# Kernel tuning notes

Measured on AMD Instinct MI355X. Metric: run time of the kernel, lower is better.

The kernel has to match this reference:

```python
import jax, jax.numpy as jnp
import numpy as np

B, T, C, H, HD = 2, 1024, 1024, 16, 64

def _l2norm(x):
    return x / jnp.maximum(jnp.linalg.norm(x, axis=-1, keepdims=True), 1e-12)

def _rms(x):
    return x * jax.lax.rsqrt(jnp.mean(x * x, axis=-1, keepdims=True) + 1e-6)

def _rope_tables(t, hd):
    inv = 1.0 / (10000.0 ** (jnp.arange(0, hd, 2, dtype=jnp.float32) / hd))
    fr = jnp.outer(jnp.arange(t, dtype=jnp.float32), inv)  # [T, hd/2]
    return jnp.cos(fr)[None, :, None, :], jnp.sin(fr)[None, :, None, :]

def _rope(x, cos, sin):
    h = x.shape[-1] // 2
    x1, x2 = x[..., :h], x[..., h:]
    return jnp.concatenate([x1 * cos + x2 * sin, -x1 * sin + x2 * cos], axis=-1)

def _qkv_heads(x, Wqkv, cos, sin):
    q, k, v = jnp.split(x @ Wqkv.T, 3, axis=-1)
    q = _rope(q.reshape(B, T, H, HD), cos, sin)
    k = _rope(k.reshape(B, T, H, HD), cos, sin)
    return q, k, v.reshape(B, T, H, HD)

def _bhtd(x):
    return jnp.swapaxes(x, 1, 2)

def _sdpa(q, k, v, scale, causal):
    s = jnp.einsum('bhqd,bhkd->bhqk', q, k) * scale
    s = jnp.where(causal, s, -jnp.inf)
    return jnp.einsum('bhqk,bhkd->bhqd', jax.nn.softmax(s, axis=-1), v)

def _hyp_attn(q, k, v, kc, causal):
    # project to Lorentz hyperboloid <x,x>_L = -k: time = sqrt(k + |x_s|^2)
    tq = jnp.sqrt(kc + jnp.sum(q * q, axis=-1, keepdims=True))  # [B,H,T,1]
    tk = jnp.sqrt(kc + jnp.sum(k * k, axis=-1, keepdims=True))
    # Lorentz inner product for all pairs, via GEMM (no [B,H,T,T,D+1] blowup)
    inner = jnp.einsum('bhqd,bhkd->bhqk', q, k) - tq * jnp.swapaxes(tk, -1, -2)
    # d(x,y) = sqrt(k) * arccosh(-<x,y>_L / k); clamp arg for numerical safety
    dist = jnp.sqrt(kc) * jnp.arccosh(jnp.maximum(-inner / kc, 1.0 + 1e-7))
    w = jnp.where(causal, 1.0 / (1e-6 + dist), -jnp.inf)
    return jnp.einsum('bhqk,bhkd->bhqd', jax.nn.softmax(w, axis=-1), v)

def _mlp(x, Wuv, Wmo, suv_eff=None):
    uv = x @ Wuv.T
    if suv_eff is not None:
        uv = suv_eff * uv
    u, v = jnp.split(uv, 2, axis=-1)
    return (u * jax.nn.silu(v)) @ Wmo.T

def _sph_skip(x, h, alpha):
    lr = jnp.abs(alpha * (0.05 * (C ** 0.5)))  # alpha * (init_value/init_scaling)
    a, b = _l2norm(x), _l2norm(h)
    return _l2norm(a + lr * (b - a))

def _euc_hyp_block(x, Wqkv, Wo, Wuv, Wmo, cos, sin, causal, kc=None):
    h = _rms(x)
    q, k, v = _qkv_heads(h, Wqkv, cos, sin)
    q, k, v = _bhtd(q), _bhtd(k), _bhtd(v)
    if kc is None:
        a = _sdpa(q, k, v, 1.0 / (C ** 0.5), causal)
    else:
        a = _hyp_attn(q, k, v, kc, causal)
    x = x + _bhtd(a).reshape(B, T, C) @ Wo.T
    x = x + _mlp(_rms(x), Wuv, Wmo)
    return x

def _sph_block(x, Wqkv, Wo, Wuv, Wmo, sqk, suv, attn_alpha, mlp_alpha, cos, sin, causal):
    q, k, v = _qkv_heads(x, Wqkv, cos, sin)
    sqk_eff = (sqk * (C ** 0.5)).reshape(1, 1, H, HD)  # sqk * init_value/init_scaling
    q = sqk_eff * _l2norm(q)
    k = sqk_eff * _l2norm(k)
    a = _sdpa(_bhtd(q), _bhtd(k), _bhtd(v), C ** 0.5, causal)
    x = _sph_skip(x, _bhtd(a).reshape(B, T, C) @ Wo.T, attn_alpha)
    x = _sph_skip(x, _mlp(x, Wuv, Wmo, suv_eff=suv * (C ** 0.5)), mlp_alpha)
    return x

def setup_inputs() -> dict:
    key = jax.random.key(0)
    ks = jax.random.split(key, 14)
    w = lambda k, shp: jax.random.normal(k, shp, jnp.float32) * 0.02
    inp = {'x': jax.random.normal(ks[0], (B, T, C), jnp.float32)}
    for i, g in enumerate(['euc', 'hyp', 'sph']):
        inp[f'Wqkv_{g}'] = w(ks[1 + 4 * i], (3 * C, C))
        inp[f'Wo_{g}'] = w(ks[2 + 4 * i], (C, C))
        inp[f'Wuv_{g}'] = w(ks[3 + 4 * i], (8 * C, C))
        inp[f'Wmo_{g}'] = w(ks[4 + 4 * i], (C, 4 * C))
    inp['k_hyp'] = jnp.ones((1, H, 1, 1), jnp.float32)
    inp['sqk'] = jnp.ones((C,), jnp.float32) / (C ** 0.5)
    inp['suv'] = jnp.ones((8 * C,), jnp.float32)
    inp['attn_alpha'] = jnp.ones((C,), jnp.float32) / (C ** 0.5)
    inp['mlp_alpha'] = jnp.ones((C,), jnp.float32) / (C ** 0.5)
    return inp

def reference(x, Wqkv_euc, Wo_euc, Wuv_euc, Wmo_euc,
              Wqkv_hyp, Wo_hyp, Wuv_hyp, Wmo_hyp, k_hyp,
              Wqkv_sph, Wo_sph, Wuv_sph, Wmo_sph,
              sqk, suv, attn_alpha, mlp_alpha):
    cos, sin = _rope_tables(T, HD)
    causal = jnp.tril(jnp.ones((T, T), dtype=bool))
    x = _euc_hyp_block(x, Wqkv_euc, Wo_euc, Wuv_euc, Wmo_euc, cos, sin, causal)
    x = _euc_hyp_block(x, Wqkv_hyp, Wo_hyp, Wuv_hyp, Wmo_hyp, cos, sin, causal, kc=k_hyp)
    x = _sph_block(x, Wqkv_sph, Wo_sph, Wuv_sph, Wmo_sph, sqk, suv, attn_alpha, mlp_alpha, cos, sin, causal)
    return x
```

## Files before the change

### kernel.cpp

```cpp
#include <hip/hip_runtime.h>
#include <stdint.h>
#include <stddef.h>

typedef __attribute__((ext_vector_type(8))) short short8;
typedef __attribute__((ext_vector_type(4))) float f32x4;
typedef unsigned short u16;
typedef unsigned int u32;

#define DEVI __device__ __forceinline__

static constexpr int T_ = 1024, C_ = 1024, M_ = 2048;

DEVI float bf2f(u16 u){ u32 x=((u32)u)<<16; float f; __builtin_memcpy(&f,&x,4); return f; }
DEVI u16 f2bf(float f){ u32 x; __builtin_memcpy(&x,&f,4); x += 0x7fffu + ((x>>16)&1u); return (u16)(x>>16); }

DEVI void gld_lds16(const u16* g, u16* l){
  __builtin_amdgcn_global_load_lds((const __attribute__((address_space(1))) void*)g,
                                   (__attribute__((address_space(3))) void*)l, 16, 0, 0);
}
DEVI f32x4 mfma16(short8 a, short8 b, f32x4 c){
  return __builtin_amdgcn_mfma_f32_16x16x32_bf16(a, b, c, 0, 0, 0);
}

__global__ void k_cast(const float* __restrict__ in, u16* __restrict__ out){
  int i = (blockIdx.x*blockDim.x + threadIdx.x)*4;
  float4 v = *(const float4*)(in+i);
  uint2 o; o.x = (u32)f2bf(v.x) | ((u32)f2bf(v.y)<<16);
  o.y = (u32)f2bf(v.z) | ((u32)f2bf(v.w)<<16);
  *(uint2*)(out+i) = o;
}

__global__ void k_tables(float* __restrict__ cosT, float* __restrict__ sinT){
  int i = blockIdx.x*256 + threadIdx.x;
  int t = i>>5, f = i&31;
  float inv = expf(-((float)f/32.f)*9.210340371976184f);
  float fr = (float)t * inv;
  cosT[i] = cosf(fr); sinT[i] = sinf(fr);
}

template<int NORM>
__global__ void k_rms(const float* __restrict__ x, u16* __restrict__ out){
  __shared__ float ps[4];
  int row = blockIdx.x, tid = threadIdx.x;
  float4 v = ((const float4*)(x + (size_t)row*C_))[tid];
  if (NORM){
    float ss = v.x*v.x+v.y*v.y+v.z*v.z+v.w*v.w;
    #pragma unroll
    for(int o=32;o>=1;o>>=1) ss += __shfl_xor(ss,o);
    if((tid&63)==0) ps[tid>>6]=ss;
    __syncthreads();
    ss = ps[0]+ps[1]+ps[2]+ps[3];
    float r = rsqrtf(ss*(1.f/C_) + 1e-6f);
    v.x*=r; v.y*=r; v.z*=r; v.w*=r;
  }
  uint2 o; o.x=(u32)f2bf(v.x)|((u32)f2bf(v.y)<<16);
  o.y=(u32)f2bf(v.z)|((u32)f2bf(v.w)<<16);
  ((uint2*)(out + (size_t)row*C_))[tid] = o;
}

template<int EPI>
__global__ __launch_bounds__(256) void k_gemm(const u16* __restrict__ A, const u16* __restrict__ Bw,
    void* __restrict__ Cout, const float* __restrict__ Res, int M, int N, int K){
  __shared__ u16 As[128*32];
  __shared__ u16 Bs[128*32];
  const int tid = threadIdx.x, w = tid>>6, lane = tid&63;
  const int bm = blockIdx.y<<7, bn = blockIdx.x<<7;
  const int wr = w>>1, wc = w&1;
  const int sr = lane>>2, sc = lane&3;
  f32x4 acc[4][4] = {};
  const u16* ga0 = A  + (size_t)(bm + w*32 + sr)*K + sc*8;
  const u16* gb0 = Bw + (size_t)(bn + w*32 + sr)*K + sc*8;
  u16* la0 = &As[(w*32)*32];
  u16* lb0 = &Bs[(w*32)*32];
  const int r16 = lane&15, ko = (lane>>4)*8;
  for (int k0=0; k0<K; k0+=32){
    __syncthreads();
    gld_lds16(ga0 + k0, la0);
    gld_lds16(ga0 + (size_t)16*K + k0, la0 + 16*32);
    gld_lds16(gb0 + k0, lb0);
    gld_lds16(gb0 + (size_t)16*K + k0, lb0 + 16*32);
    __syncthreads();
    short8 af[4], bf[4];
    #pragma unroll
    for(int mf=0;mf<4;++mf) af[mf] = *(const short8*)&As[(wr*64+mf*16+r16)*32 + ko];
    #pragma unroll
    for(int nf=0;nf<4;++nf) bf[nf] = *(const short8*)&Bs[(wc*64+nf*16+r16)*32 + ko];
    #pragma unroll
    for(int mf=0;mf<4;++mf)
      #pragma unroll
      for(int nf=0;nf<4;++nf)
        acc[mf][nf] = mfma16(af[mf], bf[nf], acc[mf][nf]);
  }
  const int rr = (lane>>4)*4;
  #pragma unroll
  for(int mf=0;mf<4;++mf){
    #pragma unroll
    for(int nf=0;nf<4;++nf){
      #pragma unroll
      for(int r=0;r<4;++r){
        size_t idx = (size_t)(bm + wr*64 + mf*16 + rr + r)*N + (bn + wc*64 + nf*16 + r16);
        float val = acc[mf][nf][r];
        if (EPI==0)      ((u16*)Cout)[idx] = f2bf(val);
        else if (EPI==1) ((float*)Cout)[idx] = Res[idx] + val;
        else             ((float*)Cout)[idx] = val;
      }
    }
  }
}

template<int SPH>
__global__ void k_ropeqk(const u16* __restrict__ qkv, const float* __restrict__ cosT,
                         const float* __restrict__ sinT, const float* __restrict__ sqk,
                         u16* __restrict__ Qb, u16* __restrict__ Kb){
  int idx = blockIdx.x*4 + (threadIdx.x>>6);
  int lane = threadIdx.x&63;
  int bh = idx>>10, t = idx&1023;
  int b = bh>>4, h = bh&15;
  size_t qa = (size_t)(b*T_ + t)*3072 + h*64 + lane;
  float qv = bf2f(qkv[qa]), kv = bf2f(qkv[qa + 1024]);
  float c = cosT[t*32 + (lane&31)], s = sinT[t*32 + (lane&31)];
  float qo = __shfl(qv, lane^32), ko2 = __shfl(kv, lane^32);
  float qr = (lane<32) ? (qv*c + qo*s) : (qv*c - qo*s);
  float kr = (lane<32) ? (kv*c + ko2*s) : (kv*c - ko2*s);
  if (SPH){
    float sq = qr*qr, sk = kr*kr;
    #pragma unroll
    for(int o=32;o>=1;o>>=1){ sq += __shfl_xor(sq,o); sk += __shfl_xor(sk,o); }
    float sc2 = sqk[h*64+lane]*32.f;
    qr = qr / fmaxf(sqrtf(sq),1e-12f) * sc2;
    kr = kr / fmaxf(sqrtf(sk),1e-12f) * sc2;
  }
  size_t oa = (size_t)bh*T_*64 + (size_t)t*64 + lane;
  Qb[oa] = f2bf(qr); Kb[oa] = f2bf(kr);
}

__global__ void k_vtrans(const u16* __restrict__ qkv, u16* __restrict__ Vt){
  __shared__ u16 tile[64][68];
  int bh = blockIdx.x, t0 = blockIdx.y*64;
  int b = bh>>4, h = bh&15;
  int tid = threadIdx.x;
  int tt = tid>>2, ch = tid&3;
  const u16* src = qkv + (size_t)(b*T_ + t0 + tt)*3072 + 2048 + h*64 + ch*16;
  short8 v0 = *(const short8*)src;
  short8 v1 = *(const short8*)(src+8);
  #pragma unroll
  for(int j=0;j<8;++j){ tile[tt][ch*16+j]=(u16)v0[j]; tile[tt][ch*16+8+j]=(u16)v1[j]; }
  __syncthreads();
  int d = tid>>2, tc = (tid&3)*16;
  short8 a, bb;
  #pragma unroll
  for(int j=0;j<8;++j){ a[j]=(short)tile[tc+j][d]; bb[j]=(short)tile[tc+8+j][d]; }
  u16* dst = Vt + ((size_t)bh*64 + d)*T_ + t0 + tc;
  *(short8*)dst = a; *(short8*)(dst+8) = bb;
}

template<int GEOM>
__global__ __launch_bounds__(64) void k_attn_split(const u16* __restrict__ Q, const u16* __restrict__ K,
    const u16* __restrict__ Vt, const float* __restrict__ khyp,
    float* __restrict__ partO, float* __restrict__ partML){
  int qt = blockIdx.x, bh = blockIdx.y, ch = blockIdx.z;
  int kend = qt*16 + 16;
  int kbeg = ch*256;
  if (kbeg >= kend) return;
  int klim = min(kbeg + 256, kend);
  __shared__ u16 P[16*32];
  int b = bh>>4, h = bh&15;
  int lane = threadIdx.x;
  int r16 = lane&15, g = lane>>4, ko = g*8;
  const u16* Qp = Q + (size_t)bh*T_*64;
  const u16* Kp = K + (size_t)bh*T_*64;
  const u16* Vp = Vt + (size_t)bh*64*T_;
  short8 qf0 = *(const short8*)&Qp[(size_t)(qt*16 + r16)*64 + ko];
  short8 qf1 = *(const short8*)&Qp[(size_t)(qt*16 + r16)*64 + 32 + ko];
  float kc=1.f, sqkc=1.f, tqr[4];
  if (GEOM==1){
    kc = khyp[h]; sqkc = sqrtf(kc);
    float ss=0;
    #pragma unroll
    for(int j=0;j<8;++j){ float a=bf2f((u16)qf0[j]); ss+=a*a; a=bf2f((u16)qf1[j]); ss+=a*a; }
    ss += __shfl_xor(ss,16); ss += __shfl_xor(ss,32);
    float tq = sqrtf(kc + ss);
    #pragma unroll
    for(int r=0;r<4;++r) tqr[r] = __shfl(tq, g*4+r);
  }
  f32x4 of[4] = {};
  float m[4], l[4];
  #pragma unroll
  for(int r=0;r<4;++r){ m[r]=-1e30f; l[r]=0.f; }
  int ntiles = (klim - kbeg + 31)>>5;
  for(int it=0; it<ntiles; ++it){
    int kt = kbeg + it*32;
    short8 kf00 = *(const short8*)&Kp[(size_t)(kt + r16)*64 + ko];
    short8 kf01 = *(const short8*)&Kp[(size_t)(kt + r16)*64 + 32 + ko];
    short8 kf10 = *(const short8*)&Kp[(size_t)(kt + 16 + r16)*64 + ko];
    short8 kf11 = *(const short8*)&Kp[(size_t)(kt + 16 + r16)*64 + 32 + ko];
    f32x4 s0={}, s1={};
    s0 = mfma16(qf0, kf00, s0); s0 = mfma16(qf1, kf01, s0);
    s1 = mfma16(qf0, kf10, s1); s1 = mfma16(qf1, kf11, s1);
    float tk0=0.f, tk1=0.f;
    if (GEOM==1){
      float ss0=0, ss1=0;
      #pragma unroll
      for(int j=0;j<8;++j){
        float a=bf2f((u16)kf00[j]); ss0+=a*a; a=bf2f((u16)kf01[j]); ss0+=a*a;
        a=bf2f((u16)kf10[j]); ss1+=a*a; a=bf2f((u16)kf11[j]); ss1+=a*a;
      }
      ss0 += __shfl_xor(ss0,16); ss0 += __shfl_xor(ss0,32);
      ss1 += __shfl_xor(ss1,16); ss1 += __shfl_xor(ss1,32);
      tk0 = sqrtf(kc+ss0); tk1 = sqrtf(kc+ss1);
    }
    float w0[4], w1[4];
    #pragma unroll
    for(int r=0;r<4;++r){
      int qg = qt*16 + g*4 + r;
      float a0, a1;
      if (GEOM==0){ a0 = s0[r]*(1.f/32.f); a1 = s1[r]*(1.f/32.f); }
      else if (GEOM==2){ a0 = s0[r]*32.f; a1 = s1[r]*32.f; }
      else {
        float z0 = (tqr[r]*tk0 - s0[r])/kc; z0 = fmaxf(z0, 1.f+1e-7f);
        float z1 = (tqr[r]*tk1 - s1[r])/kc; z1 = fmaxf(z1, 1.f+1e-7f);
        float d0 = sqkc * logf(z0 + sqrtf(z0*z0 - 1.f));
        float d1 = sqkc * logf(z1 + sqrtf(z1*z1 - 1.f));
        a0 = 1.f/(1e-6f + d0); a1 = 1.f/(1e-6f + d1);
      }
      if (kt + r16 > qg)      a0 = -1e30f;
      if (kt + 16 + r16 > qg) a1 = -1e30f;
      w0[r]=a0; w1[r]=a1;
    }
    #pragma unroll
    for(int r=0;r<4;++r){
      float mt = fmaxf(w0[r], w1[r]);
      #pragma unroll
      for(int o=1;o<16;o<<=1) mt = fmaxf(mt, __shfl_xor(mt,o));
      float mn = fmaxf(m[r], mt);
      float alpha = __expf(m[r]-mn);
      m[r]=mn;
      float p0 = __expf(w0[r]-mn), p1 = __expf(w1[r]-mn);
      float rs = p0+p1;
      #pragma unroll
      for(int o=1;o<16;o<<=1) rs += __shfl_xor(rs,o);
      l[r] = l[r]*alpha + rs;
      #pragma unroll
      for(int vb=0;vb<4;++vb) of[vb][r] *= alpha;
      P[(g*4+r)*32 + r16]      = f2bf(p0);
      P[(g*4+r)*32 + 16 + r16] = f2bf(p1);
    }
    __syncthreads();
    short8 pf = *(const short8*)&P[r16*32 + ko];
    #pragma unroll
    for(int vb=0;vb<4;++vb){
      short8 vf = *(const short8*)&Vp[(size_t)(vb*16 + r16)*T_ + kt + ko];
      of[vb] = mfma16(pf, vf, of[vb]);
    }
    __syncthreads();
  }
  size_t base = ((size_t)(bh*64 + qt)*4 + ch);
  float* po = partO + base*1024;
  #pragma unroll
  for(int vb=0;vb<4;++vb)
    #pragma unroll
    for(int r=0;r<4;++r)
      po[(g*4+r)*64 + vb*16 + r16] = of[vb][r];
  if (r16 == 0){
    #pragma unroll
    for(int r=0;r<4;++r){
      partML[(base*16 + g*4+r)*2    ] = m[r];
      partML[(base*16 + g*4+r)*2 + 1] = l[r];
    }
  }
}

__global__ __launch_bounds__(64) void k_attn_combine(const float* __restrict__ partO,
    const float* __restrict__ partML, u16* __restrict__ Oo){
  int qt = blockIdx.x, bh = blockIdx.y;
  int b = bh>>4, h = bh&15;
  int lane = threadIdx.x;
  int r16 = lane&15, g = lane>>4;
  int nch = (qt>>4) + 1;
  size_t base0 = ((size_t)(bh*64 + qt)*4);
  #pragma unroll
  for(int r=0;r<4;++r){
    int row = g*4 + r;
    float mstar = -1e30f;
    for(int c=0;c<nch;++c)
      mstar = fmaxf(mstar, partML[((base0+c)*16 + row)*2]);
    float lstar = 0.f;
    float ov[4] = {0.f,0.f,0.f,0.f};
    for(int c=0;c<nch;++c){
      float mc = partML[((base0+c)*16 + row)*2];
      float lc = partML[((base0+c)*16 + row)*2 + 1];
      float wgt = __expf(mc - mstar);
      lstar += lc * wgt;
      const float* po = partO + (base0+c)*1024 + row*64;
      #pragma unroll
      for(int vb=0;vb<4;++vb) ov[vb] += po[vb*16 + r16] * wgt;
    }
    float inv = 1.f / lstar;
    int t = qt*16 + row;
    #pragma unroll
    for(int vb=0;vb<4;++vb)
      Oo[((size_t)(b*T_ + t))*C_ + h*64 + vb*16 + r16] = f2bf(ov[vb] * inv);
  }
}

template<int SUV>
__global__ void k_silu(const u16* __restrict__ uv, const float* __restrict__ suv, u16* __restrict__ g){
  int i = blockIdx.x*256 + threadIdx.x;
  int m = i>>10, j = (i&1023)*4;
  const u16* up = uv + (size_t)m*8192 + j;
  uint2 uu = *(const uint2*)up;
  uint2 vv = *(const uint2*)(up+4096);
  float u[4] = { bf2f((u16)(uu.x&0xffff)), bf2f((u16)(uu.x>>16)), bf2f((u16)(uu.y&0xffff)), bf2f((u16)(uu.y>>16)) };
  float v[4] = { bf2f((u16)(vv.x&0xffff)), bf2f((u16)(vv.x>>16)), bf2f((u16)(vv.y&0xffff)), bf2f((u16)(vv.y>>16)) };
  float o[4];
  #pragma unroll
  for(int e=0;e<4;++e){
    float ue=u[e], ve=v[e];
    if (SUV){ ue *= suv[j+e]*32.0f; ve *= suv[4096+j+e]*32.0f; }
    o[e] = ue * (ve / (1.0f + __expf(-ve)));
  }
  uint2 oo; oo.x=(u32)f2bf(o[0])|((u32)f2bf(o[1])<<16); oo.y=(u32)f2bf(o[2])|((u32)f2bf(o[3])<<16);
  *(uint2*)(g + (size_t)m*4096 + j) = oo;
}

__global__ void k_sphskip(const float* __restrict__ x, const float* __restrict__ hh,
                          const float* __restrict__ alpha, float* __restrict__ out){
  __shared__ float red[3][4];
  int row = blockIdx.x, tid = threadIdx.x;
  float4 xv = ((const float4*)(x  + (size_t)row*C_))[tid];
  float4 hv = ((const float4*)(hh + (size_t)row*C_))[tid];
  float ssx = xv.x*xv.x+xv.y*xv.y+xv.z*xv.z+xv.w*xv.w;
  float ssh = hv.x*hv.x+hv.y*hv.y+hv.z*hv.z+hv.w*hv.w;
  #pragma unroll
  for(int o=32;o>=1;o>>=1){ ssx += __shfl_xor(ssx,o); ssh += __shfl_xor(ssh,o); }
  if((tid&63)==0){ red[0][tid>>6]=ssx; red[1][tid>>6]=ssh; }
  __syncthreads();
  ssx = red[0][0]+red[0][1]+red[0][2]+red[0][3];
  ssh = red[1][0]+red[1][1]+red[1][2]+red[1][3];
  float rx = 1.f/fmaxf(sqrtf(ssx),1e-12f), rh = 1.f/fmaxf(sqrtf(ssh),1e-12f);
  float4 al = ((const float4*)alpha)[tid];
  float y[4]; float ssy=0.f;
  { float a0=xv.x*rx, b0=hv.x*rh, lr=fabsf(al.x*1.6f); y[0]=a0+lr*(b0-a0); ssy+=y[0]*y[0]; }
  { float a0=xv.y*rx, b0=hv.y*rh, lr=fabsf(al.y*1.6f); y[1]=a0+lr*(b0-a0); ssy+=y[1]*y[1]; }
  { float a0=xv.z*rx, b0=hv.z*rh, lr=fabsf(al.z*1.6f); y[2]=a0+lr*(b0-a0); ssy+=y[2]*y[2]; }
  { float a0=xv.w*rx, b0=hv.w*rh, lr=fabsf(al.w*1.6f); y[3]=a0+lr*(b0-a0); ssy+=y[3]*y[3]; }
  #pragma unroll
  for(int o=32;o>=1;o>>=1) ssy += __shfl_xor(ssy,o);
  if((tid&63)==0) red[2][tid>>6]=ssy;
  __syncthreads();
  ssy = red[2][0]+red[2][1]+red[2][2]+red[2][3];
  float ry = 1.f/fmaxf(sqrtf(ssy),1e-12f);
  float4 o4; o4.x=y[0]*ry; o4.y=y[1]*ry; o4.z=y[2]*ry; o4.w=y[3]*ry;
  ((float4*)(out + (size_t)row*C_))[tid] = o4;
}

extern "C" void kernel_launch(void* const* d_in, const int* in_sizes, int n_in,
                              void* d_out, int out_size, void* d_ws, size_t ws_size,
                              hipStream_t stream){
  (void)n_in; (void)out_size; (void)ws_size;
  int i_khyp, sphb;
  if (in_sizes[9]==16){ i_khyp=9; sphb=10; } else { i_khyp=13; sphb=9; }
  const float* Wq[3] = {(const float*)d_in[1], (const float*)d_in[5], (const float*)d_in[sphb+0]};
  const float* Wo[3] = {(const float*)d_in[2], (const float*)d_in[6], (const float*)d_in[sphb+1]};
  const float* Wu[3] = {(const float*)d_in[3], (const float*)d_in[7], (const float*)d_in[sphb+2]};
  const float* Wm[3] = {(const float*)d_in[4], (const float*)d_in[8], (const float*)d_in[sphb+3]};
  const float* khyp = (const float*)d_in[i_khyp];
  const float* sqk  = (const float*)d_in[14];
  const float* suv  = (const float*)d_in[15];
  const float* aal  = (const float*)d_in[16];
  const float* mal  = (const float*)d_in[17];

  char* p = (char*)d_ws;
  auto alloc = [&](size_t bytes)->char*{ char* r=p; p += (bytes+255)&~(size_t)255; return r; };
  float* x    = (float*)alloc((size_t)M_*C_*4);
  float* hf32 = (float*)alloc((size_t)M_*C_*4);
  u16* h_bf   = (u16*)alloc((size_t)M_*C_*2);
  u16* qkv    = (u16*)alloc((size_t)M_*3072*2);
  u16* Qb     = (u16*)alloc((size_t)M_*1024*2);
  u16* Kb     = (u16*)alloc((size_t)M_*1024*2);
  u16* Vt     = (u16*)alloc((size_t)M_*1024*2);
  u16* att    = (u16*)alloc((size_t)M_*1024*2);
  u16* uvb    = (u16*)alloc((size_t)M_*8192*2);
  u16* gb     = (u16*)alloc((size_t)M_*4096*2);
  u16* wqb    = (u16*)alloc((size_t)3*C_*C_*2);
  u16* wob    = (u16*)alloc((size_t)C_*C_*2);
  u16* wub    = (u16*)alloc((size_t)8*C_*C_*2);
  u16* wmb    = (u16*)alloc((size_t)4*C_*C_*2);
  float* cosT = (float*)alloc((size_t)T_*32*4);
  float* sinT = (float*)alloc((size_t)T_*32*4);
  float* partO  = (float*)uvb;
  float* partML = partO + (size_t)8*1024*1024;

  hipMemcpyAsync(x, d_in[0], (size_t)M_*C_*4, hipMemcpyDeviceToDevice, stream);
  k_tables<<<T_*32/256, 256, 0, stream>>>(cosT, sinT);

  for (int gi=0; gi<3; ++gi){
    bool sph = (gi==2);
    k_cast<<<3*C_*C_/1024, 256, 0, stream>>>(Wq[gi], wqb);
    k_cast<<<  C_*C_/1024, 256, 0, stream>>>(Wo[gi], wob);
    k_cast<<<8*C_*C_/1024, 256, 0, stream>>>(Wu[gi], wub);
    k_cast<<<4*C_*C_/1024, 256, 0, stream>>>(Wm[gi], wmb);

    if (!sph) k_rms<1><<<M_,256,0,stream>>>(x, h_bf);
    else      k_rms<0><<<M_,256,0,stream>>>(x, h_bf);
    k_gemm<0><<<dim3(24,16),256,0,stream>>>(h_bf, wqb, qkv, nullptr, M_, 3072, 1024);
    if (sph) k_ropeqk<1><<<8192,256,0,stream>>>(qkv, cosT, sinT, sqk, Qb, Kb);
    else     k_ropeqk<0><<<8192,256,0,stream>>>(qkv, cosT, sinT, nullptr, Qb, Kb);
    k_vtrans<<<dim3(32,16),256,0,stream>>>(qkv, Vt);
    if (gi==0)      k_attn_split<0><<<dim3(64,32,4),64,0,stream>>>(Qb,Kb,Vt,nullptr,partO,partML);
    else if (gi==1) k_attn_split<1><<<dim3(64,32,4),64,0,stream>>>(Qb,Kb,Vt,khyp,partO,partML);
    else            k_attn_split<2><<<dim3(64,32,4),64,0,stream>>>(Qb,Kb,Vt,nullptr,partO,partML);
    k_attn_combine<<<dim3(64,32),64,0,stream>>>(partO, partML, att);

    if (!sph){
      k_gemm<1><<<dim3(8,16),256,0,stream>>>(att, wob, x, x, M_, 1024, 1024);
      k_rms<1><<<M_,256,0,stream>>>(x, h_bf);
      k_gemm<0><<<dim3(64,16),256,0,stream>>>(h_bf, wub, uvb, nullptr, M_, 8192, 1024);
      k_silu<0><<<8192,256,0,stream>>>(uvb, nullptr, gb);
      k_gemm<1><<<dim3(8,16),256,0,stream>>>(gb, wmb, x, x, M_, 1024, 4096);
    } else {
      k_gemm<2><<<dim3(8,16),256,0,stream>>>(att, wob, hf32, nullptr, M_, 1024, 1024);
      k_sphskip<<<M_,256,0,stream>>>(x, hf32, aal, x);
      k_rms<0><<<M_,256,0,stream>>>(x, h_bf);
      k_gemm<0><<<dim3(64,16),256,0,stream>>>(h_bf, wub, uvb, nullptr, M_, 8192, 1024);
      k_silu<1><<<8192,256,0,stream>>>(uvb, suv, gb);
      k_gemm<2><<<dim3(8,16),256,0,stream>>>(gb, wmb, hf32, nullptr, M_, 1024, 4096);
      k_sphskip<<<M_,256,0,stream>>>(x, hf32, mal, (float*)d_out);
    }
  }
}
```

Baseline: 1.124 ms.

## Split-K the narrow output GEMMs and merge weight casts into one launch

```diff
diff --git a/kernel.cpp b/kernel.cpp
--- a/kernel.cpp
+++ b/kernel.cpp
@@ -22,12 +22,21 @@
   return __builtin_amdgcn_mfma_f32_16x16x32_bf16(a, b, c, 0, 0, 0);
 }
 
-__global__ void k_cast(const float* __restrict__ in, u16* __restrict__ out){
-  int i = (blockIdx.x*blockDim.x + threadIdx.x)*4;
-  float4 v = *(const float4*)(in+i);
-  uint2 o; o.x = (u32)f2bf(v.x) | ((u32)f2bf(v.y)<<16);
-  o.y = (u32)f2bf(v.z) | ((u32)f2bf(v.w)<<16);
-  *(uint2*)(out+i) = o;
+__global__ void k_cast4(const float* __restrict__ q, const float* __restrict__ o,
+                        const float* __restrict__ u, const float* __restrict__ m,
+                        u16* __restrict__ qo, u16* __restrict__ oo,
+                        u16* __restrict__ uo, u16* __restrict__ mo){
+  int blk = blockIdx.x;
+  const float* src; u16* dst; int base;
+  if (blk < 3072)      { src=q; dst=qo; base=blk; }
+  else if (blk < 4096) { src=o; dst=oo; base=blk-3072; }
+  else if (blk < 12288){ src=u; dst=uo; base=blk-4096; }
+  else                 { src=m; dst=mo; base=blk-12288; }
+  size_t i = (size_t)base*1024 + threadIdx.x*4;
+  float4 v = *(const float4*)(src+i);
+  uint2 ov; ov.x = (u32)f2bf(v.x) | ((u32)f2bf(v.y)<<16);
+  ov.y = (u32)f2bf(v.z) | ((u32)f2bf(v.w)<<16);
+  *(uint2*)(dst+i) = ov;
 }
 
 __global__ void k_tables(float* __restrict__ cosT, float* __restrict__ sinT){
@@ -106,6 +115,69 @@
       }
     }
   }
+}
+
+__global__ __launch_bounds__(256) void k_gemm_sk(const u16* __restrict__ A, const u16* __restrict__ Bw,
+    float* __restrict__ partC, int M, int N, int K, int KC){
+  __shared__ u16 As[128*32];
+  __shared__ u16 Bs[128*32];
+  const int tid = threadIdx.x, w = tid>>6, lane = tid&63;
+  const int bm = blockIdx.y<<7, bn = blockIdx.x<<7;
+  const int kb = blockIdx.z*KC;
+  const int wr = w>>1, wc = w&1;
+  const int sr = lane>>2, sc = lane&3;
+  f32x4 acc[4][4] = {};
+  const u16* ga0 = A  + (size_t)(bm + w*32 + sr)*K + sc*8;
+  const u16* gb0 = Bw + (size_t)(bn + w*32 + sr)*K + sc*8;
+  u16* la0 = &As[(w*32)*32];
+  u16* lb0 = &Bs[(w*32)*32];
+  const int r16 = lane&15, ko = (lane>>4)*8;
+  for (int k0=kb; k0<kb+KC; k0+=32){
+    __syncthreads();
+    gld_lds16(ga0 + k0, la0);
+    gld_lds16(ga0 + (size_t)16*K + k0, la0 + 16*32);
+    gld_lds16(gb0 + k0, lb0);
+    gld_lds16(gb0 + (size_t)16*K + k0, lb0 + 16*32);
+    __syncthreads();
+    short8 af[4], bf[4];
+    #pragma unroll
+    for(int mf=0;mf<4;++mf) af[mf] = *(const short8*)&As[(wr*64+mf*16+r16)*32 + ko];
+    #pragma unroll
+    for(int nf=0;nf<4;++nf) bf[nf] = *(const short8*)&Bs[(wc*64+nf*16+r16)*32 + ko];
+    #pragma unroll
+    for(int mf=0;mf<4;++mf)
+      #pragma unroll
+      for(int nf=0;nf<4;++nf)
+        acc[mf][nf] = mfma16(af[mf], bf[nf], acc[mf][nf]);
+  }
+  float* pc = partC + (size_t)blockIdx.z*M*N;
+  const int rr = (lane>>4)*4;
+  #pragma unroll
+  for(int mf=0;mf<4;++mf)
+    #pragma unroll
+    for(int nf=0;nf<4;++nf)
+      #pragma unroll
+      for(int r=0;r<4;++r){
+        size_t idx = (size_t)(bm + wr*64 + mf*16 + rr + r)*N + (bn + wc*64 + nf*16 + r16);
+        pc[idx] = acc[mf][nf][r];
+      }
+}
+
+template<int RES, int NS>
+__global__ void k_skred(const float* __restrict__ partC, const float* __restrict__ Res,
+                        float* __restrict__ out, int MN){
+  int i = (blockIdx.x*256 + threadIdx.x)*4;
+  float4 s = *(const float4*)(partC + i);
+  #pragma unroll
+  for(int z=1; z<NS; ++z){
+    float4 t = *(const float4*)(partC + (size_t)z*MN + i);
+    s.x+=t.x; s.y+=t.y; s.z+=t.z; s.w+=t.w;
+  }
+  if (RES){
+    float4 rv = *(const float4*)(Res + i);
+    s.x+=rv.x; s.y+=rv.y; s.z+=rv.z; s.w+=rv.w;
+  }
+  *(float4*)(out + i) = s;
 }
 
 template<int SPH>
@@ -390,16 +462,16 @@
   float* sinT = (float*)alloc((size_t)T_*32*4);
   float* partO  = (float*)uvb;
   float* partML = partO + (size_t)8*1024*1024;
+  partML = hf32 + (size_t)7*256*1024;
+  float* partC  = (float*)uvb;
 
   hipMemcpyAsync(x, d_in[0], (size_t)M_*C_*4, hipMemcpyDeviceToDevice, stream);
   k_tables<<<T_*32/256, 256, 0, stream>>>(cosT, sinT);
 
+  const int MN = M_*C_;
   for (int gi=0; gi<3; ++gi){
     bool sph = (gi==2);
-    k_cast<<<3*C_*C_/1024, 256, 0, stream>>>(Wq[gi], wqb);
-    k_cast<<<  C_*C_/1024, 256, 0, stream>>>(Wo[gi], wob);
-    k_cast<<<8*C_*C_/1024, 256, 0, stream>>>(Wu[gi], wub);
-    k_cast<<<4*C_*C_/1024, 256, 0, stream>>>(Wm[gi], wmb);
+    k_cast4<<<16384, 256, 0, stream>>>(Wq[gi], Wo[gi], Wu[gi], Wm[gi], wqb, wob, wub, wmb);
 
     if (!sph) k_rms<1><<<M_,256,0,stream>>>(x, h_bf);
     else      k_rms<0><<<M_,256,0,stream>>>(x, h_bf);
@@ -413,18 +485,22 @@
     k_attn_combine<<<dim3(64,32),64,0,stream>>>(partO, partML, att);
 
     if (!sph){
-      k_gemm<1><<<dim3(8,16),256,0,stream>>>(att, wob, x, x, M_, 1024, 1024);
+      k_gemm_sk<<<dim3(8,16,2),256,0,stream>>>(att, wob, partC, M_, 1024, 1024, 512);
+      k_skred<1,2><<<MN/1024,256,0,stream>>>(partC, x, x, MN);
       k_rms<1><<<M_,256,0,stream>>>(x, h_bf);
       k_gemm<0><<<dim3(64,16),256,0,stream>>>(h_bf, wub, uvb, nullptr, M_, 8192, 1024);
       k_silu<0><<<8192,256,0,stream>>>(uvb, nullptr, gb);
-      k_gemm<1><<<dim3(8,16),256,0,stream>>>(gb, wmb, x, x, M_, 1024, 4096);
+      k_gemm_sk<<<dim3(8,16,4),256,0,stream>>>(gb, wmb, partC, M_, 1024, 4096, 1024);
+      k_skred<1,4><<<MN/1024,256,0,stream>>>(partC, x, x, MN);
     } else {
-      k_gemm<2><<<dim3(8,16),256,0,stream>>>(att, wob, hf32, nullptr, M_, 1024, 1024);
+      k_gemm_sk<<<dim3(8,16,2),256,0,stream>>>(att, wob, partC, M_, 1024, 1024, 512);
+      k_skred<0,2><<<MN/1024,256,0,stream>>>(partC, nullptr, hf32, MN);
       k_sphskip<<<M_,256,0,stream>>>(x, hf32, aal, x);
       k_rms<0><<<M_,256,0,stream>>>(x, h_bf);
       k_gemm<0><<<dim3(64,16),256,0,stream>>>(h_bf, wub, uvb, nullptr, M_, 8192, 1024);
       k_silu<1><<<8192,256,0,stream>>>(uvb, suv, gb);
-      k_gemm<2><<<dim3(8,16),256,0,stream>>>(gb, wmb, hf32, nullptr, M_, 1024, 4096);
+      k_gemm_sk<<<dim3(8,16,4),256,0,stream>>>(gb, wmb, partC, M_, 1024, 4096, 1024);
+      k_skred<0,4><<<MN/1024,256,0,stream>>>(partC, nullptr, hf32, MN);
       k_sphskip<<<M_,256,0,stream>>>(x, hf32, mal, (float*)d_out);
     }
   }
```

Measured after the change: 960.8 us. 1.17x faster.
